# Optimization experiments

Measured on AMD Instinct MI355X. Metric: run time of the kernel, lower is better.

## Reference

```python
import jax, jax.numpy as jnp
import numpy as np

H = 8                 # num_heads
SCALE = 25.0          # self.scale
SIM_THRESH = 0.75
CONF_SIM_THRESH = 0.99


def _l2n(x):
    return x / jnp.linalg.norm(x, axis=-1, keepdims=True)


def setup_inputs() -> dict:
    key = jax.random.key(0)
    ks = jax.random.split(key, 10)
    B, N1, N2, C = 1, 512, 2048, 1024
    s = 0.02
    return {
        'x_cls': jax.random.normal(ks[0], (B, N2, C), jnp.float32),
        'x_reg': jax.random.normal(ks[1], (B, N2, C), jnp.float32),
        'cls_score': jax.random.uniform(ks[2], (N2,), dtype=jnp.float32),
        'fg_score': jax.random.uniform(ks[3], (N2,), dtype=jnp.float32),
        'W_q_cls': jax.random.normal(ks[4], (C, C), jnp.float32) * s,
        'W_kv_cls': jax.random.normal(ks[5], (C, 2 * C), jnp.float32) * s,
        'W_q_reg': jax.random.normal(ks[6], (C, C), jnp.float32) * s,
        'W_kv_reg': jax.random.normal(ks[7], (C, 2 * C), jnp.float32) * s,
        'W_lin': jax.random.normal(ks[8], (2 * C, 2 * C), jnp.float32) * s,
        'b_lin': jnp.zeros((2 * C,), jnp.float32),
        'W_lin_reg': jax.random.normal(ks[9], (2 * C, 2 * C), jnp.float32) * s,
        'b_lin_reg': jnp.zeros((2 * C,), jnp.float32),
        'local_preds_num': 512,
    }


def _forward(x_cls, x_reg, cls_score, fg_score, W_q_cls, W_kv_cls, W_q_reg, W_kv_reg,
             W_lin, b_lin, W_lin_reg, b_lin_reg, N1):
    B, N2, C = x_cls.shape
    hd = C // H
    # QKV projections (torch Linear with bias=False; weights stored [in,out])
    q_cls = (x_cls[:, :N1] @ W_q_cls).reshape(B, N1, H, hd).transpose(0, 2, 1, 3)   # [B,H,N1,hd]
    kv = (x_cls @ W_kv_cls).reshape(B, N2, 2, H, hd).transpose(2, 0, 3, 1, 4)
    k_cls, v_cls = kv[0], kv[1]                                                      # [B,H,N2,hd]
    q_reg = (x_reg[:, :N1] @ W_q_reg).reshape(B, N1, H, hd).transpose(0, 2, 1, 3)
    kv = (x_reg @ W_kv_reg).reshape(B, N2, 2, H, hd).transpose(2, 0, 3, 1, 4)
    k_reg, v_reg = kv[0], kv[1]
    # L2 normalization of q, k and of v for raw similarity
    q_cls, k_cls = _l2n(q_cls), _l2n(k_cls)
    q_reg, k_reg = _l2n(q_reg), _l2n(k_reg)
    v_cls_n, v_reg_n = _l2n(v_cls), _l2n(v_reg)
    # per-key score broadcast over [1,H,N1,N2] (use_mask=False path)
    cs = cls_score.reshape(1, 1, 1, N2)
    # raw value-value similarity
    attn_cls_raw = jnp.einsum('bhqd,bhkd->bhqk', v_cls_n[:, :, :N1], v_cls_n)        # [B,H,N1,N2]
    attn_reg_raw = jnp.einsum('bhqd,bhkd->bhqk', v_reg_n[:, :, :N1], v_reg_n)
    # blended softmax attention (attn_drop=0 -> identity)
    attn_cls = jax.nn.softmax(jnp.einsum('bhqd,bhkd->bhqk', q_cls, k_cls) * SCALE * cs, axis=-1)
    attn_reg = jax.nn.softmax(jnp.einsum('bhqd,bhkd->bhqk', q_reg, k_reg) * SCALE, axis=-1)
    attn = (attn_cls + attn_reg) * 0.5
    # attended features + original local values, then output linears
    x = jnp.einsum('bhqk,bhkd->bhqd', attn, v_cls).transpose(0, 2, 1, 3).reshape(B, N1, C)
    x_ori = v_cls[:, :, :N1].transpose(0, 2, 1, 3).reshape(B, N1, C)
    out_cls = jnp.concatenate([x, x_ori], axis=-1) @ W_lin + b_lin                   # [B,N1,2C]
    xr = jnp.einsum('bhqk,bhkd->bhqd', attn, v_reg).transpose(0, 2, 1, 3).reshape(B, N1, C)
    xr_ori = v_reg[:, :, :N1].transpose(0, 2, 1, 3).reshape(B, N1, C)
    out_reg = jnp.concatenate([xr, xr_ori], axis=-1) @ W_lin_reg + b_lin_reg         # reconf=True
    # ave branch: similarity-masked renormalized second-round averaging (batch 0)
    sim_mask = (attn_cls_raw.sum(axis=1)[0] / H > SIM_THRESH).astype(x_cls.dtype)    # [N1,N2]
    obj_mask = (attn_reg_raw.sum(axis=1)[0] / H > CONF_SIM_THRESH).astype(x_cls.dtype)
    sim_round2 = jax.nn.softmax(attn.sum(axis=1)[0] / H, axis=-1)
    sim_round2 = sim_mask * sim_round2
    sim_round2 = sim_round2 / sim_round2.sum(axis=-1, keepdims=True)
    obj_w = obj_mask * sim_round2
    obj_w = obj_w / obj_w.sum(axis=-1, keepdims=True)
    support_cls = v_cls.transpose(0, 2, 1, 3).reshape(B, N2, C)[0]                   # [N2,C]
    support_reg = v_reg.transpose(0, 2, 1, 3).reshape(B, N2, C)[0]
    cls_feature = jnp.concatenate([sim_round2 @ support_cls, out_cls[0]], axis=-1)   # [N1,3C]
    reg_feature = jnp.concatenate([obj_w @ support_reg, out_reg[0]], axis=-1)        # [N1,3C]
    return cls_feature, reg_feature


def reference(x_cls, x_reg, cls_score, fg_score, W_q_cls, W_kv_cls, W_q_reg, W_kv_reg,
              W_lin, b_lin, W_lin_reg, b_lin_reg, local_preds_num):
    return _forward(x_cls, x_reg, cls_score, fg_score, W_q_cls, W_kv_cls, W_q_reg,
                    W_kv_reg, W_lin, b_lin, W_lin_reg, b_lin_reg, local_preds_num)
```

## Files before the change

kernel.cpp:

```cpp
#include <hip/hip_runtime.h>

typedef _Float16 half8 __attribute__((ext_vector_type(8)));
typedef _Float16 half4v __attribute__((ext_vector_type(4)));
typedef float f32x4 __attribute__((ext_vector_type(4)));

#define GLD16(gptr, lptr) \
    __builtin_amdgcn_global_load_lds((const __attribute__((address_space(1))) void*)(gptr), \
                                     (__attribute__((address_space(3))) void*)(lptr), 16, 0, 0)

#define WAIT_VM3   0x0F73
#define WAIT_VM0   0x0F70
#define WAIT_LGKM0 0xC07F

struct GD {
    const _Float16* A; const _Float16* B; void* C;
    const float* colScale;
    long sAh, sAg, sBh, sBg, sSplit, sCh, sCg;
    int lda, ldb, ldc, K, SK, hmask, hshift;
    int ahx, outHalf, csMode, nx, ny;
    float alpha;
};

__global__ __launch_bounds__(512, 4)
void hgemm3(GD d0, GD d1, int zSplit)
{
    const bool second = (int)blockIdx.z >= zSplit;
    const GD& d = second ? d1 : d0;
    const int bz = second ? (int)blockIdx.z - zSplit : (int)blockIdx.z;
    if ((int)blockIdx.x >= d.nx || (int)blockIdx.y >= d.ny) return;

    __shared__ uint4 smem[4608];
    char* sb = (char*)smem;
    const int tid = threadIdx.x;
    const int w = tid >> 6, l = tid & 63;
    const int m0 = blockIdx.y << 8, n0 = blockIdx.x << 7;
    const int wm = (w >> 1) << 6, wn = (w & 1) << 6;
    const int kq = l >> 4, lm = l & 15;

    const int zz = bz / d.SK, s = bz - zz * d.SK;
    const int h = d.ahx ? (int)blockIdx.x : (zz & d.hmask);
    const int g = d.ahx ? zz : (zz >> d.hshift);
    const _Float16* A = d.A + (long)h * d.sAh + (long)g * d.sAg;
    const _Float16* B = d.B + (long)h * d.sBh + (long)g * d.sBg;
    const long Coff = (long)s * d.sSplit + (long)h * d.sCh + (long)g * d.sCg;
    const int kper = d.K / d.SK, kbeg = s * kper;
    const int NT = kper >> 5;

    const int rS = (w << 4) + (l >> 2);
    const int cS = (l & 3) ^ ((l >> 3) & 3);
    const _Float16* gA0 = A + (long)(m0 + rS) * d.lda + kbeg + cS * 8;
    const _Float16* gB0 = B + (long)(n0 + rS) * d.ldb + kbeg + cS * 8;
    const int lo = w * 1024 + l * 16;

    auto stage = [&](int t) {
        char* dst = sb + (t % 3) * 24576;
        GLD16(gA0 + t * 32,                     dst + lo);
        GLD16(gA0 + (long)128 * d.lda + t * 32, dst + 8192 + lo);
        GLD16(gB0 + t * 32,                     dst + 16384 + lo);
    };

    f32x4 acc[4][4] = {};
    stage(0);
    if (NT > 1) stage(1);
    if (NT > 1) __builtin_amdgcn_s_waitcnt(WAIT_VM3);
    else        __builtin_amdgcn_s_waitcnt(WAIT_VM0);
    __builtin_amdgcn_s_barrier();

    const int sw16 = ((kq ^ ((lm >> 1) & 3)) << 4);
    for (int t = 0; t < NT; ++t) {
        const char* cb = sb + (t % 3) * 24576;
        half8 af[4], bfr[4];
        const char* pa = cb + (wm + lm) * 64 + sw16;
        const char* pb = cb + 16384 + (wn + lm) * 64 + sw16;
        #pragma unroll
        for (int i = 0; i < 4; ++i) {
            af[i]  = *(const half8*)(pa + i * 1024);
            bfr[i] = *(const half8*)(pb + i * 1024);
        }
        #pragma unroll
        for (int mi = 0; mi < 4; ++mi)
            #pragma unroll
            for (int ni = 0; ni < 4; ++ni)
                acc[mi][ni] = __builtin_amdgcn_mfma_f32_16x16x32_f16(af[mi], bfr[ni], acc[mi][ni], 0, 0, 0);
        __builtin_amdgcn_s_waitcnt(WAIT_LGKM0);
        if (t + 2 < NT) { stage(t + 2); __builtin_amdgcn_s_waitcnt(WAIT_VM3); }
        else if (t + 1 < NT) __builtin_amdgcn_s_waitcnt(WAIT_VM0);
        __builtin_amdgcn_s_barrier();
    }

    const int rbase = m0 + wm + kq * 4;
    #pragma unroll
    for (int mi = 0; mi < 4; ++mi) {
        #pragma unroll
        for (int ni = 0; ni < 4; ++ni) {
            const int col = n0 + wn + ni * 16 + lm;
            float cs = d.alpha;
            if (d.csMode == 1 || (d.csMode == 2 && g == 0)) cs *= d.colScale[col];
            #pragma unroll
            for (int r = 0; r < 4; ++r) {
                const long row = rbase + mi * 16 + r;
                const float v = acc[mi][ni][r] * cs;
                const long off = Coff + row * d.ldc + col;
                if (d.outHalf) ((_Float16*)d.C)[off] = (_Float16)v;
                else           ((float*)d.C)[off] = v;
            }
        }
    }
}

static GD mkgd(const _Float16* A, const _Float16* B, void* C, const float* cscale,
               long sAh, long sAg, long sBh, long sBg, long sSplit, long sCh, long sCg,
               int lda, int ldb, int ldc, int K, int SK, int hmask, int hshift,
               int ahx, int outHalf, int csMode, int nx, int ny, float alpha)
{
    GD d; d.A=A; d.B=B; d.C=C; d.colScale=cscale;
    d.sAh=sAh; d.sAg=sAg; d.sBh=sBh; d.sBg=sBg; d.sSplit=sSplit; d.sCh=sCh; d.sCg=sCg;
    d.lda=lda; d.ldb=ldb; d.ldc=ldc; d.K=K; d.SK=SK; d.hmask=hmask; d.hshift=hshift;
    d.ahx=ahx; d.outHalf=outHalf; d.csMode=csMode; d.nx=nx; d.ny=ny; d.alpha=alpha;
    return d;
}

__global__ __launch_bounds__(256)
void cast_f2h(const float* __restrict__ s0, const float* __restrict__ s1,
              _Float16* __restrict__ d, int n4)
{
    const int i = blockIdx.x * 256 + threadIdx.x;
    const float* s = blockIdx.y ? s1 : s0;
    const float4 v = ((const float4*)s)[i];
    half4v o;
    o.x = (_Float16)v.x; o.y = (_Float16)v.y; o.z = (_Float16)v.z; o.w = (_Float16)v.w;
    ((half4v*)(d + (size_t)blockIdx.y * n4 * 4))[i] = o;
}

__global__ __launch_bounds__(256)
void prep_transpose(const float* __restrict__ Wq_c, const float* __restrict__ Wq_r,
                    const float* __restrict__ Wkv_c, const float* __restrict__ Wkv_r,
                    const float* __restrict__ Wl_c, const float* __restrict__ Wl_r,
                    _Float16* __restrict__ WqT, _Float16* __restrict__ WkvT,
                    _Float16* __restrict__ WlinT)
{
    __shared__ float t[32][33];
    const int z = blockIdx.z;
    const float* src; _Float16* dst; int ldsrc, lddst, nx, ky;
    switch (z) {
        case 0: src=Wq_c;  dst=WqT;            ldsrc=1024; lddst=1024; nx=32; ky=32; break;
        case 1: src=Wq_r;  dst=WqT+1048576;    ldsrc=1024; lddst=1024; nx=32; ky=32; break;
        case 2: src=Wkv_c; dst=WkvT;           ldsrc=2048; lddst=1024; nx=64; ky=32; break;
        case 3: src=Wkv_r; dst=WkvT+2097152;   ldsrc=2048; lddst=1024; nx=64; ky=32; break;
        case 4: src=Wl_c;  dst=WlinT;          ldsrc=2048; lddst=2048; nx=64; ky=64; break;
        default:src=Wl_r;  dst=WlinT+4194304;  ldsrc=2048; lddst=2048; nx=64; ky=64; break;
    }
    if ((int)blockIdx.x >= nx || (int)blockIdx.y >= ky) return;
    const int n0 = blockIdx.x << 5, k0 = blockIdx.y << 5;
    const int tx = threadIdx.x & 31, ty = threadIdx.x >> 5;
    #pragma unroll
    for (int j = ty; j < 32; j += 8)
        t[j][tx] = src[(size_t)(k0 + j) * ldsrc + n0 + tx];
    __syncthreads();
    #pragma unroll
    for (int j = ty; j < 32; j += 8)
        dst[(size_t)(n0 + j) * lddst + k0 + tx] = (_Float16)t[tx][j];
}

__global__ __launch_bounds__(256)
void phase3(const _Float16* __restrict__ qh, const _Float16* __restrict__ kvh,
            _Float16* __restrict__ qn, _Float16* __restrict__ kn,
            _Float16* __restrict__ vn, _Float16* __restrict__ x_ori,
            _Float16* __restrict__ vT)
{
    __shared__ float t[32][33];
    const int b = blockIdx.x;
    if (b < 2048) {
        const int vid = b * 4 + (threadIdx.x >> 6);
        const int lane = threadIdx.x & 63;
        const int g = vid >> 12, rr = vid & 4095, row = rr >> 3, hh = rr & 7;
        const size_t o = (size_t)g * 524288 + (size_t)row * 1024 + hh * 128 + lane * 2;
        const float a = (float)qh[o], bb = (float)qh[o + 1];
        float ss = a * a + bb * bb;
        #pragma unroll
        for (int d = 32; d > 0; d >>= 1) ss += __shfl_xor(ss, d, 64);
        const float inv = rsqrtf(ss);
        qn[o] = (_Float16)(a * inv); qn[o + 1] = (_Float16)(bb * inv);
    } else if (b < 18432) {
        const int vid = (b - 2048) * 4 + (threadIdx.x >> 6);
        const int lane = threadIdx.x & 63;
        const int half_ = vid >> 15;
        const int r15 = vid & 32767;
        const int g = r15 >> 14, rr = r15 & 16383, row = rr >> 3, hh = rr & 7;
        const size_t so = (size_t)g * 4194304 + (size_t)row * 2048
                        + half_ * 1024 + hh * 128 + lane * 2;
        const float a = (float)kvh[so], bb = (float)kvh[so + 1];
        float ss = a * a + bb * bb;
        #pragma unroll
        for (int d = 32; d > 0; d >>= 1) ss += __shfl_xor(ss, d, 64);
        const float inv = rsqrtf(ss);
        const size_t dofs = (size_t)g * 2097152 + (size_t)row * 1024 + hh * 128 + lane * 2;
        _Float16* dp = (half_ ? vn : kn) + dofs;
        dp[0] = (_Float16)(a * inv); dp[1] = (_Float16)(bb * inv);
        if (half_ == 1 && row < 512) {
            _Float16* xo = x_ori + (size_t)g * 524288 + (size_t)row * 1024 + hh * 128 + lane * 2;
            xo[0] = (_Float16)a; xo[1] = (_Float16)bb;
        }
    } else {
        const int vb = b - 18432;
        const int g = vb >> 11, r = vb & 2047;
        const int n0 = (r & 31) << 5, k0 = (r >> 5) << 5;
        const int tx = threadIdx.x & 31, ty = threadIdx.x >> 5;
        const _Float16* s0 = kvh + (size_t)g * 4194304 + 1024;
        #pragma unroll
        for (int j = ty; j < 32; j += 8)
            t[j][tx] = (float)s0[(size_t)(k0 + j) * 2048 + n0 + tx];
        __syncthreads();
        _Float16* d = vT + (size_t)g * 2097152;
        #pragma unroll
        for (int j = ty; j < 32; j += 8)
            d[(size_t)(n0 + j) * 2048 + k0 + tx] = (_Float16)t[tx][j];
    }
}

template<int OP>
__device__ __forceinline__ float bred(float v, float* lds)
{
    #pragma unroll
    for (int o = 32; o > 0; o >>= 1) {
        const float u = __shfl_xor(v, o, 64);
        v = OP ? fmaxf(v, u) : v + u;
    }
    __syncthreads();
    if ((threadIdx.x & 63) == 0) lds[threadIdx.x >> 6] = v;
    __syncthreads();
    return OP ? fmaxf(fmaxf(lds[0], lds[1]), fmaxf(lds[2], lds[3]))
              : lds[0] + lds[1] + lds[2] + lds[3];
}

__global__ __launch_bounds__(256)
void sb2_kernel(const _Float16* __restrict__ S16, const float* __restrict__ simPart,
                _Float16* __restrict__ attn,
                _Float16* __restrict__ wc, _Float16* __restrict__ wr)
{
    __shared__ float lds[4];
    const int q = blockIdx.x, t = threadIdx.x;
    float asum[8] = {};
    for (int hh = 0; hh < 8; ++hh) {
        const size_t rb = (size_t)(hh * 512 + q) * 2048;
        float vc[8], vr[8];
        float mc = -1e30f, mr = -1e30f;
        #pragma unroll
        for (int j = 0; j < 8; ++j) {
            vc[j] = (float)S16[rb + t + 256 * j];
            vr[j] = (float)S16[8388608 + rb + t + 256 * j];
            mc = fmaxf(mc, vc[j]); mr = fmaxf(mr, vr[j]);
        }
        mc = bred<1>(mc, lds);
        mr = bred<1>(mr, lds);
        float sc = 0.f, sr = 0.f;
        #pragma unroll
        for (int j = 0; j < 8; ++j) {
            vc[j] = expf(vc[j] - mc); sc += vc[j];
            vr[j] = expf(vr[j] - mr); sr += vr[j];
        }
        sc = bred<0>(sc, lds);
        sr = bred<0>(sr, lds);
        const float ic = 0.5f / sc, ir = 0.5f / sr;
        #pragma unroll
        for (int j = 0; j < 8; ++j) {
            const float a = vc[j] * ic + vr[j] * ir;
            attn[rb + t + 256 * j] = (_Float16)a;
            asum[j] += a;
        }
    }
    float mx = -1e30f;
    #pragma unroll
    for (int j = 0; j < 8; ++j) { asum[j] *= 0.125f; mx = fmaxf(mx, asum[j]); }
    mx = bred<1>(mx, lds);
    float em[8], emo[8];
    float s1 = 0.f, s2 = 0.f;
    const size_t qb = (size_t)q * 2048;
    #pragma unroll
    for (int j = 0; j < 8; ++j) {
        const size_t o = qb + t + 256 * j;
        const float sim = simPart[o];
        const float reg = simPart[1048576 + o];
        const float e = expf(asum[j] - mx);
        const float m  = sim > 0.75f ? 1.f : 0.f;
        const float mo = reg > 0.99f ? 1.f : 0.f;
        em[j] = e * m; emo[j] = e * m * mo;
        s1 += em[j]; s2 += emo[j];
    }
    s1 = bred<0>(s1, lds);
    s2 = bred<0>(s2, lds);
    const float i1 = 1.f / s1, i2 = 1.f / s2;
    #pragma unroll
    for (int j = 0; j < 8; ++j) {
        wc[qb + t + 256 * j] = (_Float16)(em[j] * i1);
        wr[qb + t + 256 * j] = (_Float16)(emo[j] * i2);
    }
}

__global__ __launch_bounds__(256)
void build_xcat(const float* __restrict__ xcatPart, const _Float16* __restrict__ x_ori,
                _Float16* __restrict__ xcat)
{
    const int idx = blockIdx.x * 256 + threadIdx.x;
    const int j = idx & 2047;
    const int n = (idx >> 11) & 511;
    const int g = idx >> 20;
    _Float16 v;
    if (j < 1024) {
        float a = 0.f;
        #pragma unroll
        for (int s = 0; s < 4; ++s)
            a += xcatPart[(size_t)s * 1048576 + (size_t)g * 524288 + n * 1024 + j];
        v = (_Float16)a;
    } else {
        v = x_ori[(size_t)g * 524288 + (size_t)n * 1024 + (j - 1024)];
    }
    xcat[idx] = v;
}

__global__ __launch_bounds__(256)
void finalize(const float* __restrict__ avePart, const float* __restrict__ outPart,
              const float* __restrict__ b_lin, const float* __restrict__ b_lin_reg,
              float* __restrict__ out)
{
    const int idx = blockIdx.x * 256 + threadIdx.x;
    const int c = idx % 3072;
    const int r = (idx / 3072) & 511;
    const int g = idx / (3072 * 512);
    float v;
    if (c < 1024) {
        v = 0.f;
        #pragma unroll
        for (int s = 0; s < 4; ++s)
            v += avePart[(size_t)s * 1048576 + (size_t)g * 524288 + r * 1024 + c];
    } else {
        const int cc = c - 1024;
        v = (g ? b_lin_reg : b_lin)[cc];
        #pragma unroll
        for (int s = 0; s < 4; ++s)
            v += outPart[(size_t)s * 2097152 + (size_t)g * 1048576 + r * 2048 + cc];
    }
    out[idx] = v;
}

extern "C" void kernel_launch(void* const* d_in, const int* in_sizes, int n_in,
                              void* d_out, int out_size, void* d_ws, size_t ws_size,
                              hipStream_t stream)
{
    const float* x_cls     = (const float*)d_in[0];
    const float* x_reg     = (const float*)d_in[1];
    const float* cls_score = (const float*)d_in[2];
    const float* W_q_cls   = (const float*)d_in[4];
    const float* W_kv_cls  = (const float*)d_in[5];
    const float* W_q_reg   = (const float*)d_in[6];
    const float* W_kv_reg  = (const float*)d_in[7];
    const float* W_lin     = (const float*)d_in[8];
    const float* b_lin     = (const float*)d_in[9];
    const float* W_lin_reg = (const float*)d_in[10];
    const float* b_lin_reg = (const float*)d_in[11];
    float* out = (float*)d_out;

    if (ws_size < (size_t)124 * 1048576) return;

    char* W = (char*)d_ws;
    auto at = [&](size_t mb) { return (void*)(W + mb * 1048576); };
    _Float16* WlinT   = (_Float16*)at(0);
    _Float16* vT      = (_Float16*)at(16);
    _Float16* x_ori   = (_Float16*)at(24);
    _Float16* w_c     = (_Float16*)at(26);
    _Float16* w_r     = (_Float16*)at(28);
    _Float16* qn      = (_Float16*)at(30);
    _Float16* kvh     = (_Float16*)at(32);
    float*    simPart = (float*)at(32);
    float*    outPart = (float*)at(32);
    _Float16* qh      = (_Float16*)at(64);
    _Float16* WqT     = (_Float16*)at(66);
    _Float16* WkvT    = (_Float16*)at(70);
    _Float16* kn      = (_Float16*)at(66);
    _Float16* vn      = (_Float16*)at(74);
    _Float16* attn_h  = (_Float16*)at(66);
    _Float16* xbf     = (_Float16*)at(82);
    _Float16* xcat16  = (_Float16*)at(82);
    _Float16* S16     = (_Float16*)at(90);
    float*    xcatPart= (float*)at(90);
    float*    avePart = (float*)at(106);

    cast_f2h<<<dim3(2048, 2), 256, 0, stream>>>(x_cls, x_reg, xbf, 524288);
    prep_transpose<<<dim3(64, 64, 6), 256, 0, stream>>>(
        W_q_cls, W_q_reg, W_kv_cls, W_kv_reg, W_lin, W_lin_reg, WqT, WkvT, WlinT);

    {
        GD q  = mkgd(xbf, WqT, qh, nullptr,
                     0, 2097152, 0, 1048576, 0, 0, 524288,
                     1024, 1024, 1024, 1024, 1, 0, 0, 0, 1, 0, 8, 2, 1.f);
        GD kv = mkgd(xbf, WkvT, kvh, nullptr,
                     0, 2097152, 0, 2097152, 0, 0, 4194304,
                     1024, 1024, 2048, 1024, 1, 0, 0, 0, 1, 0, 16, 8, 1.f);
        hgemm3<<<dim3(16, 8, 4), 512, 0, stream>>>(q, kv, 2);
    }

    phase3<<<22528, 256, 0, stream>>>(qh, kvh, qn, kn, vn, x_ori, vT);

    {
        GD vs = mkgd(vn, vn, simPart, nullptr,
                     0, 2097152, 0, 2097152, 0, 0, 1048576,
                     1024, 1024, 2048, 1024, 1, 0, 0, 0, 0, 0, 16, 2, 0.125f);
        GD sc = mkgd(qn, kn, S16, cls_score,
                     128, 524288, 128, 2097152, 0, 1048576, 8388608,
                     1024, 1024, 2048, 128, 1, 7, 3, 0, 1, 2, 16, 2, 25.f);
        hgemm3<<<dim3(16, 2, 18), 512, 0, stream>>>(vs, sc, 2);
    }

    sb2_kernel<<<512, 256, 0, stream>>>(S16, simPart, attn_h, w_c, w_r);

    {
        GD av = mkgd(attn_h, vT, xcatPart, nullptr,
                     1048576, 0, 0, 2097152, 1048576, 0, 524288,
                     2048, 2048, 1024, 2048, 4, 0, 0, 1, 0, 0, 8, 2, 1.f);
        GD ae = mkgd(w_c, vT, avePart, nullptr,
                     0, 1048576, 0, 2097152, 1048576, 0, 524288,
                     2048, 2048, 1024, 2048, 4, 0, 0, 0, 0, 0, 8, 2, 1.f);
        hgemm3<<<dim3(8, 2, 16), 512, 0, stream>>>(av, ae, 8);
    }

    build_xcat<<<8192, 256, 0, stream>>>(xcatPart, x_ori, xcat16);

    {
        GD ol = mkgd(xcat16, WlinT, outPart, nullptr,
                     0, 1048576, 0, 4194304, 2097152, 0, 1048576,
                     2048, 2048, 2048, 2048, 4, 0, 0, 0, 0, 0, 16, 2, 1.f);
        hgemm3<<<dim3(16, 2, 8), 512, 0, stream>>>(ol, ol, 8);
    }

    finalize<<<12288, 256, 0, stream>>>(avePart, outPart, b_lin, b_lin_reg, out);
}
```

Before: 305.9 us.

## Fuse per-head L2 normalization and V transpose into projection GEMM epilogue

Removes the separate phase3 kernel by normalizing q, k and v rows inside the QKV GEMM epilogue. Each 128-column block tile equals one head, so per-row sums of squares are reduced with shuffles and shared memory. The epilogue also writes x_ori and the transposed V directly. This avoids writing the fp16 qh/kvh intermediates, reading them back, and one kernel launch. The cost is a heavier epilogue with an extra barrier and a strided transposed store, and the workspace layout is reshuffled.

```diff
diff --git a/kernel.cpp b/kernel.cpp
--- a/kernel.cpp
+++ b/kernel.cpp
@@ -15,9 +15,10 @@
 struct GD {
     const _Float16* A; const _Float16* B; void* C;
     const float* colScale;
+    _Float16 *vnp, *vtp, *xop;
     long sAh, sAg, sBh, sBg, sSplit, sCh, sCg;
     int lda, ldb, ldc, K, SK, hmask, hshift;
-    int ahx, outHalf, csMode, nx, ny;
+    int ahx, outHalf, csMode, nx, ny, normMode;
     float alpha;
 };
 
@@ -88,23 +89,97 @@
         __builtin_amdgcn_s_barrier();
     }
 
-    const int rbase = m0 + wm + kq * 4;
+    if (d.normMode == 0) {
+        const int rbase = m0 + wm + kq * 4;
+        #pragma unroll
+        for (int mi = 0; mi < 4; ++mi) {
+            #pragma unroll
+            for (int ni = 0; ni < 4; ++ni) {
+                const int col = n0 + wn + ni * 16 + lm;
+                float cs = d.alpha;
+                if (d.csMode == 1 || (d.csMode == 2 && g == 0)) cs *= d.colScale[col];
+                #pragma unroll
+                for (int r = 0; r < 4; ++r) {
+                    const long row = rbase + mi * 16 + r;
+                    const float v = acc[mi][ni][r] * cs;
+                    const long off = Coff + row * d.ldc + col;
+                    if (d.outHalf) ((_Float16*)d.C)[off] = (_Float16)v;
+                    else           ((float*)d.C)[off] = v;
+                }
+            }
+        }
+        return;
+    }
+
+    float* part = (float*)sb;
+    float ssq[4][4];
+    #pragma unroll
+    for (int mi = 0; mi < 4; ++mi)
+        #pragma unroll
+        for (int r = 0; r < 4; ++r) {
+            float sq = 0.f;
+            #pragma unroll
+            for (int ni = 0; ni < 4; ++ni) { const float v = acc[mi][ni][r]; sq += v * v; }
+            sq += __shfl_xor(sq, 1, 64);
+            sq += __shfl_xor(sq, 2, 64);
+            sq += __shfl_xor(sq, 4, 64);
+            sq += __shfl_xor(sq, 8, 64);
+            ssq[mi][r] = sq;
+        }
+    if (lm == 0) {
+        #pragma unroll
+        for (int mi = 0; mi < 4; ++mi)
+            #pragma unroll
+            for (int r = 0; r < 4; ++r)
+                part[(w & 1) * 256 + wm + kq * 4 + mi * 16 + r] = ssq[mi][r];
+    }
+    __syncthreads();
+
     #pragma unroll
     for (int mi = 0; mi < 4; ++mi) {
         #pragma unroll
-        for (int ni = 0; ni < 4; ++ni) {
-            const int col = n0 + wn + ni * 16 + lm;
-            float cs = d.alpha;
-            if (d.csMode == 1 || (d.csMode == 2 && g == 0)) cs *= d.colScale[col];
+        for (int r = 0; r < 4; ++r) {
+            const int rl = wm + kq * 4 + mi * 16 + r;
+            const float inv = rsqrtf(part[rl] + part[256 + rl]);
+            const long rg = m0 + rl;
+            if (d.normMode == 1) {
+                #pragma unroll
+                for (int ni = 0; ni < 4; ++ni) {
+                    const int col = n0 + wn + ni * 16 + lm;
+                    ((_Float16*)d.C)[(long)g * 524288 + rg * 1024 + col] =
+                        (_Float16)(acc[mi][ni][r] * inv);
+                }
+            } else if (n0 < 1024) {
+                #pragma unroll
+                for (int ni = 0; ni < 4; ++ni) {
+                    const int col = n0 + wn + ni * 16 + lm;
+                    ((_Float16*)d.C)[(long)g * 2097152 + rg * 1024 + col] =
+                        (_Float16)(acc[mi][ni][r] * inv);
+                }
+            } else {
+                #pragma unroll
+                for (int ni = 0; ni < 4; ++ni) {
+                    const int nL = n0 - 1024 + wn + ni * 16 + lm;
+                    d.vnp[(long)g * 2097152 + rg * 1024 + nL] =
+                        (_Float16)(acc[mi][ni][r] * inv);
+                    if (rg < 512)
+                        d.xop[(long)g * 524288 + rg * 1024 + nL] = (_Float16)acc[mi][ni][r];
+                }
+            }
+        }
+    }
+    if (d.normMode == 2 && n0 >= 1024) {
+        #pragma unroll
+        for (int mi = 0; mi < 4; ++mi)
             #pragma unroll
-            for (int r = 0; r < 4; ++r) {
-                const long row = rbase + mi * 16 + r;
-                const float v = acc[mi][ni][r] * cs;
-                const long off = Coff + row * d.ldc + col;
-                if (d.outHalf) ((_Float16*)d.C)[off] = (_Float16)v;
-                else           ((float*)d.C)[off] = v;
+            for (int ni = 0; ni < 4; ++ni) {
+                const int nL = n0 - 1024 + wn + ni * 16 + lm;
+                half4v t;
+                t.x = (_Float16)acc[mi][ni][0]; t.y = (_Float16)acc[mi][ni][1];
+                t.z = (_Float16)acc[mi][ni][2]; t.w = (_Float16)acc[mi][ni][3];
+                *(half4v*)(d.vtp + (long)g * 2097152 + (long)nL * 2048
+                           + m0 + wm + kq * 4 + mi * 16) = t;
             }
-        }
     }
 }
 
@@ -114,9 +189,11 @@
                int ahx, int outHalf, int csMode, int nx, int ny, float alpha)
 {
     GD d; d.A=A; d.B=B; d.C=C; d.colScale=cscale;
+    d.vnp=nullptr; d.vtp=nullptr; d.xop=nullptr;
     d.sAh=sAh; d.sAg=sAg; d.sBh=sBh; d.sBg=sBg; d.sSplit=sSplit; d.sCh=sCh; d.sCg=sCg;
     d.lda=lda; d.ldb=ldb; d.ldc=ldc; d.K=K; d.SK=SK; d.hmask=hmask; d.hshift=hshift;
-    d.ahx=ahx; d.outHalf=outHalf; d.csMode=csMode; d.nx=nx; d.ny=ny; d.alpha=alpha;
+    d.ahx=ahx; d.outHalf=outHalf; d.csMode=csMode; d.nx=nx; d.ny=ny; d.normMode=0;
+    d.alpha=alpha;
     return d;
 }
 
@@ -160,62 +237,6 @@
     #pragma unroll
     for (int j = ty; j < 32; j += 8)
         dst[(size_t)(n0 + j) * lddst + k0 + tx] = (_Float16)t[tx][j];
-}
-
-__global__ __launch_bounds__(256)
-void phase3(const _Float16* __restrict__ qh, const _Float16* __restrict__ kvh,
-            _Float16* __restrict__ qn, _Float16* __restrict__ kn,
-            _Float16* __restrict__ vn, _Float16* __restrict__ x_ori,
-            _Float16* __restrict__ vT)
-{
-    __shared__ float t[32][33];
-    const int b = blockIdx.x;
-    if (b < 2048) {
-        const int vid = b * 4 + (threadIdx.x >> 6);
-        const int lane = threadIdx.x & 63;
-        const int g = vid >> 12, rr = vid & 4095, row = rr >> 3, hh = rr & 7;
-        const size_t o = (size_t)g * 524288 + (size_t)row * 1024 + hh * 128 + lane * 2;
-        const float a = (float)qh[o], bb = (float)qh[o + 1];
-        float ss = a * a + bb * bb;
-        #pragma unroll
-        for (int d = 32; d > 0; d >>= 1) ss += __shfl_xor(ss, d, 64);
-        const float inv = rsqrtf(ss);
-        qn[o] = (_Float16)(a * inv); qn[o + 1] = (_Float16)(bb * inv);
-    } else if (b < 18432) {
-        const int vid = (b - 2048) * 4 + (threadIdx.x >> 6);
-        const int lane = threadIdx.x & 63;
-        const int half_ = vid >> 15;
-        const int r15 = vid & 32767;
-        const int g = r15 >> 14, rr = r15 & 16383, row = rr >> 3, hh = rr & 7;
-        const size_t so = (size_t)g * 4194304 + (size_t)row * 2048
-                        + half_ * 1024 + hh * 128 + lane * 2;
-        const float a = (float)kvh[so], bb = (float)kvh[so + 1];
-        float ss = a * a + bb * bb;
-        #pragma unroll
-        for (int d = 32; d > 0; d >>= 1) ss += __shfl_xor(ss, d, 64);
-        const float inv = rsqrtf(ss);
-        const size_t dofs = (size_t)g * 2097152 + (size_t)row * 1024 + hh * 128 + lane * 2;
-        _Float16* dp = (half_ ? vn : kn) + dofs;
-        dp[0] = (_Float16)(a * inv); dp[1] = (_Float16)(bb * inv);
-        if (half_ == 1 && row < 512) {
-            _Float16* xo = x_ori + (size_t)g * 524288 + (size_t)row * 1024 + hh * 128 + lane * 2;
-            xo[0] = (_Float16)a; xo[1] = (_Float16)bb;
-        }
-    } else {
-        const int vb = b - 18432;
-        const int g = vb >> 11, r = vb & 2047;
-        const int n0 = (r & 31) << 5, k0 = (r >> 5) << 5;
-        const int tx = threadIdx.x & 31, ty = threadIdx.x >> 5;
-        const _Float16* s0 = kvh + (size_t)g * 4194304 + 1024;
-        #pragma unroll
-        for (int j = ty; j < 32; j += 8)
-            t[j][tx] = (float)s0[(size_t)(k0 + j) * 2048 + n0 + tx];
-        __syncthreads();
-        _Float16* d = vT + (size_t)g * 2097152;
-        #pragma unroll
-        for (int j = ty; j < 32; j += 8)
-            d[(size_t)(n0 + j) * 2048 + k0 + tx] = (_Float16)t[tx][j];
-    }
 }
 
 template<int OP>
@@ -370,36 +391,34 @@
     _Float16* w_c     = (_Float16*)at(26);
     _Float16* w_r     = (_Float16*)at(28);
     _Float16* qn      = (_Float16*)at(30);
-    _Float16* kvh     = (_Float16*)at(32);
     float*    simPart = (float*)at(32);
     float*    outPart = (float*)at(32);
-    _Float16* qh      = (_Float16*)at(64);
-    _Float16* WqT     = (_Float16*)at(66);
-    _Float16* WkvT    = (_Float16*)at(70);
-    _Float16* kn      = (_Float16*)at(66);
-    _Float16* vn      = (_Float16*)at(74);
-    _Float16* attn_h  = (_Float16*)at(66);
-    _Float16* xbf     = (_Float16*)at(82);
-    _Float16* xcat16  = (_Float16*)at(82);
-    _Float16* S16     = (_Float16*)at(90);
-    float*    xcatPart= (float*)at(90);
-    float*    avePart = (float*)at(106);
+    _Float16* kn      = (_Float16*)at(40);
+    _Float16* vn      = (_Float16*)at(48);
+    _Float16* attn_h  = (_Float16*)at(40);
+    _Float16* xbf     = (_Float16*)at(56);
+    _Float16* WqT     = (_Float16*)at(64);
+    _Float16* xcat16  = (_Float16*)at(64);
+    _Float16* WkvT    = (_Float16*)at(68);
+    _Float16* S16     = (_Float16*)at(76);
+    float*    xcatPart= (float*)at(76);
+    float*    avePart = (float*)at(92);
 
     cast_f2h<<<dim3(2048, 2), 256, 0, stream>>>(x_cls, x_reg, xbf, 524288);
     prep_transpose<<<dim3(64, 64, 6), 256, 0, stream>>>(
         W_q_cls, W_q_reg, W_kv_cls, W_kv_reg, W_lin, W_lin_reg, WqT, WkvT, WlinT);
 
     {
-        GD q  = mkgd(xbf, WqT, qh, nullptr,
-                     0, 2097152, 0, 1048576, 0, 0, 524288,
-                     1024, 1024, 1024, 1024, 1, 0, 0, 0, 1, 0, 8, 2, 1.f);
-        GD kv = mkgd(xbf, WkvT, kvh, nullptr,
-                     0, 2097152, 0, 2097152, 0, 0, 4194304,
-                     1024, 1024, 2048, 1024, 1, 0, 0, 0, 1, 0, 16, 8, 1.f);
+        GD q  = mkgd(xbf, WqT, qn, nullptr,
+                     0, 2097152, 0, 1048576, 0, 0, 0,
+                     1024, 1024, 1024, 1024, 1, 0, 0, 1, 0, 0, 8, 2, 1.f);
+        q.normMode = 1;
+        GD kv = mkgd(xbf, WkvT, kn, nullptr,
+                     0, 2097152, 0, 2097152, 0, 0, 0,
+                     1024, 1024, 1024, 1024, 1, 0, 0, 1, 0, 0, 16, 8, 1.f);
+        kv.normMode = 2; kv.vnp = vn; kv.vtp = vT; kv.xop = x_ori;
         hgemm3<<<dim3(16, 8, 4), 512, 0, stream>>>(q, kv, 2);
     }
-
-    phase3<<<22528, 256, 0, stream>>>(qh, kvh, qn, kn, vn, x_ori, vT);
 
     {
         GD vs = mkgd(vn, vn, simPart, nullptr,
```

Result: faster. 296.0 us (-3.2%).
